# Optimization experiments

Hardware: AMD Instinct MI355X
Metric: run time of the kernel (lower is better)

The kernel has to match this reference:

```python
import jax, jax.numpy as jnp
import numpy as np

HIER = [1, 9, 90, 900, 18000]   # hierchy_struc = get_HTS_strc(...).get_pred_loc()
N = sum(HIER)                    # total time series = attention batch dim
L = len(HIER)                    # levelcount = attention sequence dim
T = 168                          # time_step
HOR = 24                         # horizon
U = 256                          # units[0] = units[1] = units[2] = d_model
NB = 3                           # nblock
NH = 4                           # heads
DK = U // NH


def setup_inputs() -> dict:
    key = jax.random.key(0)
    ks = jax.random.split(key, 10)
    g = lambda k, shape, fan: jax.random.normal(k, shape, jnp.float32) / np.sqrt(fan)
    return {
        "x": jax.random.normal(ks[0], (N, T), jnp.float32),
        "Wl": g(ks[1], (NB, U, T), T),     # fcLSTM (bias=False)
        "Wl1": g(ks[2], (NB, U, U), U),    # fcLSTM1 (bias=False)
        "Wq": g(ks[3], (NB, U, U), U),
        "bq": jnp.zeros((NB, U), jnp.float32),
        "Wk": g(ks[4], (NB, U, U), U),
        "bk": jnp.zeros((NB, U), jnp.float32),
        "Wv": g(ks[5], (NB, U, U), U),
        "bv": jnp.zeros((NB, U), jnp.float32),
        "Wo": g(ks[6], (NB, U, U), U),     # linears[-1] of MultiHeadedAttention
        "bo": jnp.zeros((NB, U), jnp.float32),
        "W20": g(ks[7], (NB, T, U), U),    # fc20 (bias=False)
        "Wfc2": g(ks[8], (HOR, T), T),     # fc2 (bias=False)
        "level_ids": jnp.asarray(np.repeat(np.arange(L), HIER), jnp.int32),
    }


def reference(x, Wl, Wl1, Wq, bq, Wk, bk, Wv, bv, Wo, bo, W20, Wfc2, level_ids):
    softplus = jax.nn.softplus
    n = x.shape[0]
    # get_attmask: TS i (belonging to hierarchy level l) keeps only query row l,
    # applied POST-softmax (mask_matrix=None branch of attention()).
    qmask = jax.nn.one_hot(level_ids, L, dtype=x.dtype)            # (N, L)

    def heads(Y):  # (N, L, U) -> (N, NH, L, DK)
        return Y.reshape(n, L, NH, DK).transpose(0, 2, 1, 3)

    for b in range(NB):
        h = softplus(x @ Wl[b].T)                                  # acf(fcLSTM(x))
        h = softplus(h @ Wl1[b].T)                                 # acf(fcLSTM1(.))
        X = jnp.broadcast_to(h[:, None, :], (n, L, U))             # per-level token stream
        q = heads(X @ Wq[b].T + bq[b])
        k = heads(X @ Wk[b].T + bk[b])
        v = heads(X @ Wv[b].T + bv[b])
        scores = jnp.einsum('nhqd,nhkd->nhqk', q, k) / np.sqrt(DK)  # (N, NH, L, L)
        p = jax.nn.softmax(scores, axis=-1)
        p = p * qmask[:, None, :, None]                             # hierarchical scatter mask
        o = jnp.einsum('nhqk,nhkd->nhqd', p, v)
        o = o.transpose(0, 2, 1, 3).reshape(n, L, U)                # merge heads
        o = o @ Wo[b].T + bo[b]                                     # linears[-1]
        y = o[jnp.arange(n), level_ids]                             # own-level row per TS (N, U)
        x = x + y @ W20[b].T                                        # fc20 + residual, (N, T)
    return x @ Wfc2.T                                               # fc2 -> (N, HOR)
```

## Files before the change

### kernel.cpp

```cpp
#include <hip/hip_runtime.h>
#include <hip/hip_bf16.h>
#include <math.h>

#define N_TS   19000
#define RPB    80
#define NBLKS  238
#define T_DIM  168
#define T_PAD  192
#define U_DIM  256
#define NBLK   3
#define HOR    24

using bf16 = __hip_bfloat16;
typedef short v8s __attribute__((ext_vector_type(8)));
typedef float v4f __attribute__((ext_vector_type(4)));

#define MFMA(a, b, c) __builtin_amdgcn_mfma_f32_16x16x32_bf16((a), (b), (c), 0, 0, 0)

#define BAR() do { asm volatile("s_waitcnt lgkmcnt(0)" ::: "memory"); \
                   __builtin_amdgcn_s_barrier(); } while (0)

__device__ __forceinline__ float softplus_f(float z) {
    return fmaxf(z, 0.0f) + __logf(1.0f + __expf(-fabsf(z)));
}
__device__ __forceinline__ unsigned pack2bf(float a, float b) {
    __hip_bfloat162 t = __float22bfloat162_rn(make_float2(a, b));
    return *(unsigned*)&t;
}
__device__ __forceinline__ short f2bf_s(float x) {
    bf16 h = __float2bfloat16(x); return *(short*)&h;
}
__device__ __forceinline__ v8s make_v8(float4 f0, float4 f1) {
    v8s r;
    r[0] = f2bf_s(f0.x); r[1] = f2bf_s(f0.y); r[2] = f2bf_s(f0.z); r[3] = f2bf_s(f0.w);
    r[4] = f2bf_s(f1.x); r[5] = f2bf_s(f1.y); r[6] = f2bf_s(f1.z); r[7] = f2bf_s(f1.w);
    return r;
}

__global__ __launch_bounds__(256) void wprep(
    const float* __restrict__ Wl, const float* __restrict__ Wl1,
    const float* __restrict__ Wv, const float* __restrict__ bv,
    const float* __restrict__ Wo, const float* __restrict__ bo,
    const float* __restrict__ W20, const float* __restrict__ Wfc2,
    bf16* __restrict__ Wlb, bf16* __restrict__ Wl1b, bf16* __restrict__ Wvob,
    bf16* __restrict__ W20b, bf16* __restrict__ Wfc2b, float* __restrict__ bvo)
{
    const int blk = blockIdx.x, j = threadIdx.x;
    if (blk < 192) {
        const int b = blk / 64, n0 = (blk % 64) * 4;
        const float* wo0 = Wo + (size_t)(b * 256 + n0 + 0) * 256;
        const float* wo1 = Wo + (size_t)(b * 256 + n0 + 1) * 256;
        const float* wo2 = Wo + (size_t)(b * 256 + n0 + 2) * 256;
        const float* wo3 = Wo + (size_t)(b * 256 + n0 + 3) * 256;
        const float* Wv_b = Wv + (size_t)b * 65536;
        float a0 = 0.f, a1 = 0.f, a2 = 0.f, a3 = 0.f;
        #pragma unroll 4
        for (int t = 0; t < 256; ++t) {
            float v = Wv_b[(size_t)t * 256 + j];
            a0 = fmaf(wo0[t], v, a0); a1 = fmaf(wo1[t], v, a1);
            a2 = fmaf(wo2[t], v, a2); a3 = fmaf(wo3[t], v, a3);
        }
        Wvob[(size_t)(b * 256 + n0 + 0) * 256 + j] = __float2bfloat16(a0);
        Wvob[(size_t)(b * 256 + n0 + 1) * 256 + j] = __float2bfloat16(a1);
        Wvob[(size_t)(b * 256 + n0 + 2) * 256 + j] = __float2bfloat16(a2);
        Wvob[(size_t)(b * 256 + n0 + 3) * 256 + j] = __float2bfloat16(a3);

        __shared__ float4 red[256];
        const float bvv = bv[b * 256 + j];
        red[j] = make_float4(wo0[j] * bvv, wo1[j] * bvv, wo2[j] * bvv, wo3[j] * bvv);
        __syncthreads();
        for (int s = 128; s > 0; s >>= 1) {
            if (j < s) {
                float4 x0 = red[j], x1 = red[j + s];
                red[j] = make_float4(x0.x + x1.x, x0.y + x1.y, x0.z + x1.z, x0.w + x1.w);
            }
            __syncthreads();
        }
        if (j == 0) {
            float4 r0 = red[0];
            bvo[b * 256 + n0 + 0] = r0.x + bo[b * 256 + n0 + 0];
            bvo[b * 256 + n0 + 1] = r0.y + bo[b * 256 + n0 + 1];
            bvo[b * 256 + n0 + 2] = r0.z + bo[b * 256 + n0 + 2];
            bvo[b * 256 + n0 + 3] = r0.w + bo[b * 256 + n0 + 3];
        }
    } else if (blk < 960) {
        const int idx = blk - 192, b = idx >> 8, r = idx & 255;
        if (j < T_PAD)
            Wlb[(size_t)(b * 256 + r) * T_PAD + j] =
                __float2bfloat16(j < T_DIM ? Wl[(size_t)(b * 256 + r) * T_DIM + j] : 0.f);
    } else if (blk < 1728) {
        const int idx = blk - 960, b = idx >> 8, r = idx & 255;
        Wl1b[(size_t)(b * 256 + r) * 256 + j] =
            __float2bfloat16(Wl1[(size_t)(b * 256 + r) * 256 + j]);
    } else if (blk < 2304) {
        const int idx = blk - 1728, b = idx / T_PAD, r = idx % T_PAD;
        W20b[(size_t)(b * T_PAD + r) * 256 + j] =
            __float2bfloat16(r < T_DIM ? W20[(size_t)(b * T_DIM + r) * 256 + j] : 0.f);
    } else {
        const int r = blk - 2304;
        if (j < T_PAD)
            Wfc2b[r * T_PAD + j] =
                __float2bfloat16((r < HOR && j < T_DIM) ? Wfc2[r * T_DIM + j] : 0.f);
    }
}

template<int NKS, int NI>
__device__ __forceinline__ void loadW(v8s (&dst)[16], const bf16* __restrict__ W,
                                      int ld, int rowA, int rowB, int kq)
{
    #pragma unroll
    for (int i = 0; i < NI; ++i) {
        const int r = (i == 0) ? rowA : rowB;
        #pragma unroll
        for (int ks = 0; ks < NKS; ++ks)
            dst[i * NKS + ks] = *(const v8s*)&W[(size_t)r * ld + ks * 32 + 8 * kq];
    }
}

template<int NKS, bool SP, bool BIAS>
__device__ __forceinline__ void computeH(const v8s (&wreg)[16],
    const char* src, char* dst, const float* __restrict__ bias,
    int w, int r16, int kq, int swz)
{
    v4f acc[2][5] = {};
    #pragma unroll
    for (int ks = 0; ks < NKS; ++ks)
        #pragma unroll
        for (int j = 0; j < 5; ++j) {
            v8s bfr = *(const v8s*)(src + (16 * j + r16) * 512 + ((64 * ks + 16 * kq) ^ swz));
            acc[0][j] = MFMA(wreg[0 * NKS + ks], bfr, acc[0][j]);
            acc[1][j] = MFMA(wreg[1 * NKS + ks], bfr, acc[1][j]);
        }
    #pragma unroll
    for (int i = 0; i < 2; ++i) {
        const int c0 = 32 * w + 16 * i + 4 * kq;
        float4 bb = make_float4(0.f, 0.f, 0.f, 0.f);
        if (BIAS) bb = *(const float4*)&bias[c0];
        #pragma unroll
        for (int j = 0; j < 5; ++j) {
            float v0 = acc[i][j][0], v1 = acc[i][j][1], v2 = acc[i][j][2], v3 = acc[i][j][3];
            if (BIAS) { v0 += bb.x; v1 += bb.y; v2 += bb.z; v3 += bb.w; }
            if (SP) { v0 = softplus_f(v0); v1 = softplus_f(v1);
                      v2 = softplus_f(v2); v3 = softplus_f(v3); }
            *(uint2*)(dst + (16 * j + r16) * 512 + ((2 * c0) ^ swz)) =
                make_uint2(pack2bf(v0, v1), pack2bf(v2, v3));
        }
    }
}

__global__ __launch_bounds__(512, 2) void fused_net(
    const bf16* __restrict__ Wlb, const bf16* __restrict__ Wl1b,
    const bf16* __restrict__ Wvob, const bf16* __restrict__ W20b,
    const bf16* __restrict__ Wfc2b, const float* __restrict__ bvo,
    const float* __restrict__ x, float* __restrict__ out)
{
    __shared__ __align__(16) bf16  hA[RPB * 256];
    __shared__ __align__(16) bf16  hB[RPB * 256];
    __shared__ __align__(16) float hX[RPB * 192];

    const int tid  = threadIdx.x;
    const int lane = tid & 63, w = tid >> 6;
    const int r16  = lane & 15, kq = lane >> 4;
    const int swz  = (r16 & 7) << 4;
    const int bm   = blockIdx.x * RPB;

    v8s wE[16], wO[16];

    loadW<6, 2>(wE, Wlb, T_PAD, 32 * w + r16, 32 * w + 16 + r16, kq);

    for (int u = tid; u < RPB * 48; u += 512) {
        const int r = u / 48, q = u - r * 48;
        const int gr = bm + r;
        float4 v = make_float4(0.f, 0.f, 0.f, 0.f);
        if (gr < N_TS && q < 42)
            v = *(const float4*)&x[(size_t)gr * T_DIM + 4 * q];
        const int sr = (r & 7) << 4;
        *(float4*)((char*)hX + r * 768 + ((16 * q) ^ sr)) = v;
        *(uint2*)((char*)hB + r * 512 + ((8 * q) ^ sr)) =
            make_uint2(pack2bf(v.x, v.y), pack2bf(v.z, v.w));
    }
    BAR();

    for (int b = 0; b < NBLK; ++b) {
        loadW<8, 2>(wO, Wl1b + (size_t)b * 65536, 256,
                    32 * w + r16, 32 * w + 16 + r16, kq);
        computeH<6, true, false>(wE, (const char*)hB, (char*)hA, nullptr, w, r16, kq, swz);
        BAR();

        loadW<8, 2>(wE, Wvob + (size_t)b * 65536, 256,
                    32 * w + r16, 32 * w + 16 + r16, kq);
        computeH<8, true, false>(wO, (const char*)hA, (char*)hB, nullptr, w, r16, kq, swz);
        BAR();

        {
            const bf16* W4 = W20b + (size_t)b * T_PAD * 256;
            if (w < 4) loadW<8, 2>(wO, W4, 256, 16 * (2 * w) + r16, 16 * (2 * w + 1) + r16, kq);
            else       loadW<8, 1>(wO, W4, 256, 16 * (8 + w - 4) + r16, 0, kq);
        }
        computeH<8, false, true>(wE, (const char*)hB, (char*)hA, bvo + b * 256, w, r16, kq, swz);
        BAR();

        if (b < NBLK - 1) {
            loadW<6, 2>(wE, Wlb + (size_t)(b + 1) * 256 * T_PAD, T_PAD,
                        32 * w + r16, 32 * w + 16 + r16, kq);
        } else {
            #pragma unroll
            for (int ks = 0; ks < 6; ++ks)
                wE[ks] = *(const v8s*)&Wfc2b[(size_t)(16 * (w & 1) + r16) * T_PAD + ks * 32 + 8 * kq];
        }
        {
            const int ti0 = (w < 4) ? 2 * w : 8 + (w - 4);
            v4f acc[2][5] = {};
            #pragma unroll
            for (int ks = 0; ks < 8; ++ks)
                #pragma unroll
                for (int j = 0; j < 5; ++j) {
                    v8s bfr = *(const v8s*)((const char*)hA + (16 * j + r16) * 512 +
                                            ((64 * ks + 16 * kq) ^ swz));
                    acc[0][j] = MFMA(wO[ks], bfr, acc[0][j]);
                    if (w < 4) acc[1][j] = MFMA(wO[8 + ks], bfr, acc[1][j]);
                }
            #pragma unroll
            for (int i = 0; i < 2; ++i) {
                if (i == 1 && w >= 4) continue;
                const int c0 = 16 * (ti0 + i) + 4 * kq;
                #pragma unroll
                for (int j = 0; j < 5; ++j) {
                    const int row = 16 * j + r16;
                    char* pX = (char*)hX + row * 768 + ((4 * c0) ^ swz);
                    float4 v = *(float4*)pX;
                    v.x += acc[i][j][0]; v.y += acc[i][j][1];
                    v.z += acc[i][j][2]; v.w += acc[i][j][3];
                    *(float4*)pX = v;
                    *(uint2*)((char*)hB + row * 512 + ((2 * c0) ^ swz)) =
                        make_uint2(pack2bf(v.x, v.y), pack2bf(v.z, v.w));
                }
            }
        }
        BAR();
    }

    for (int u = w; u < 10; u += 8) {
        const int j = u >> 1;
        v4f acc = {};
        #pragma unroll
        for (int ks = 0; ks < 6; ++ks) {
            const char* base = (const char*)hX + (16 * j + r16) * 768;
            const int   u0   = 128 * ks + 32 * kq;
            float4 f0 = *(const float4*)(base + (u0 ^ swz));
            float4 f1 = *(const float4*)(base + ((u0 + 16) ^ swz));
            v8s xv = make_v8(f0, f1);
            acc = MFMA(wE[ks], xv, acc);
        }
        const int grow = bm + 16 * j + r16;
        const int col  = 16 * (u & 1) + 4 * kq;
        if (grow < N_TS && col < HOR)
            *(float4*)&out[(size_t)grow * HOR + col] =
                make_float4(acc[0], acc[1], acc[2], acc[3]);
    }
}

extern "C" void kernel_launch(void* const* d_in, const int* in_sizes, int n_in,
                              void* d_out, int out_size, void* d_ws, size_t ws_size,
                              hipStream_t stream) {
    const float* x    = (const float*)d_in[0];
    const float* Wl   = (const float*)d_in[1];
    const float* Wl1  = (const float*)d_in[2];
    const float* Wv   = (const float*)d_in[7];
    const float* bv   = (const float*)d_in[8];
    const float* Wo   = (const float*)d_in[9];
    const float* bo   = (const float*)d_in[10];
    const float* W20  = (const float*)d_in[11];
    const float* Wfc2 = (const float*)d_in[12];
    float* out = (float*)d_out;

    char* p = (char*)d_ws;
    auto carve = [&](size_t bytes) { char* q = p; p += (bytes + 255) & ~(size_t)255; return q; };
    bf16*  Wlb   = (bf16*)carve((size_t)NBLK * 256 * T_PAD * 2);
    bf16*  Wl1b  = (bf16*)carve((size_t)NBLK * 256 * 256 * 2);
    bf16*  Wvob  = (bf16*)carve((size_t)NBLK * 256 * 256 * 2);
    bf16*  W20b  = (bf16*)carve((size_t)NBLK * T_PAD * 256 * 2);
    bf16*  Wfc2b = (bf16*)carve((size_t)32 * T_PAD * 2);
    float* bvo   = (float*)carve((size_t)NBLK * 256 * 4);

    wprep<<<dim3(2336), dim3(256), 0, stream>>>(
        Wl, Wl1, Wv, bv, Wo, bo, W20, Wfc2, Wlb, Wl1b, Wvob, W20b, Wfc2b, bvo);
    fused_net<<<dim3(NBLKS), dim3(512), 0, stream>>>(
        Wlb, Wl1b, Wvob, W20b, Wfc2b, bvo, x, out);
}
```

Baseline: 167.8 us.

## Shrink row tile to 32 and drop weight double-buffering for higher occupancy

The per-block row tile drops from 80 to 32 rows, so there are more blocks and less LDS per block. The two weight register buffers (wE/wO) are merged into one, removing the prefetch of the next stage's weights during the current compute. The launch bound is raised to 4 blocks per CU. The aim is to trade the explicit software prefetch for more occupancy to hide latency, but each weight fragment is now reused across fewer rows, so global/L2 weight traffic rises about 2.5x.

```diff
diff --git a/kernel.cpp b/kernel.cpp
--- a/kernel.cpp
+++ b/kernel.cpp
@@ -3,8 +3,8 @@
 #include <math.h>
 
 #define N_TS   19000
-#define RPB    80
-#define NBLKS  238
+#define RPB    32
+#define NBLKS  594
 #define T_DIM  168
 #define T_PAD  192
 #define U_DIM  256
@@ -122,11 +122,11 @@
     const char* src, char* dst, const float* __restrict__ bias,
     int w, int r16, int kq, int swz)
 {
-    v4f acc[2][5] = {};
+    v4f acc[2][2] = {};
     #pragma unroll
     for (int ks = 0; ks < NKS; ++ks)
         #pragma unroll
-        for (int j = 0; j < 5; ++j) {
+        for (int j = 0; j < 2; ++j) {
             v8s bfr = *(const v8s*)(src + (16 * j + r16) * 512 + ((64 * ks + 16 * kq) ^ swz));
             acc[0][j] = MFMA(wreg[0 * NKS + ks], bfr, acc[0][j]);
             acc[1][j] = MFMA(wreg[1 * NKS + ks], bfr, acc[1][j]);
@@ -137,7 +137,7 @@
         float4 bb = make_float4(0.f, 0.f, 0.f, 0.f);
         if (BIAS) bb = *(const float4*)&bias[c0];
         #pragma unroll
-        for (int j = 0; j < 5; ++j) {
+        for (int j = 0; j < 2; ++j) {
             float v0 = acc[i][j][0], v1 = acc[i][j][1], v2 = acc[i][j][2], v3 = acc[i][j][3];
             if (BIAS) { v0 += bb.x; v1 += bb.y; v2 += bb.z; v3 += bb.w; }
             if (SP) { v0 = softplus_f(v0); v1 = softplus_f(v1);
@@ -148,7 +148,7 @@
     }
 }
 
-__global__ __launch_bounds__(512, 2) void fused_net(
+__global__ __launch_bounds__(512, 4) void fused_net(
     const bf16* __restrict__ Wlb, const bf16* __restrict__ Wl1b,
     const bf16* __restrict__ Wvob, const bf16* __restrict__ W20b,
     const bf16* __restrict__ Wfc2b, const float* __restrict__ bvo,
@@ -164,9 +164,7 @@
     const int swz  = (r16 & 7) << 4;
     const int bm   = blockIdx.x * RPB;
 
-    v8s wE[16], wO[16];
-
-    loadW<6, 2>(wE, Wlb, T_PAD, 32 * w + r16, 32 * w + 16 + r16, kq);
+    v8s wreg[16];
 
     for (int u = tid; u < RPB * 48; u += 512) {
         const int r = u / 48, q = u - r * 48;
@@ -182,50 +180,42 @@
     BAR();
 
     for (int b = 0; b < NBLK; ++b) {
-        loadW<8, 2>(wO, Wl1b + (size_t)b * 65536, 256,
+        loadW<6, 2>(wreg, Wlb + (size_t)b * 256 * T_PAD, T_PAD,
                     32 * w + r16, 32 * w + 16 + r16, kq);
-        computeH<6, true, false>(wE, (const char*)hB, (char*)hA, nullptr, w, r16, kq, swz);
-        BAR();
-
-        loadW<8, 2>(wE, Wvob + (size_t)b * 65536, 256,
+        computeH<6, true, false>(wreg, (const char*)hB, (char*)hA, nullptr, w, r16, kq, swz);
+        BAR();
+
+        loadW<8, 2>(wreg, Wl1b + (size_t)b * 65536, 256,
                     32 * w + r16, 32 * w + 16 + r16, kq);
-        computeH<8, true, false>(wO, (const char*)hA, (char*)hB, nullptr, w, r16, kq, swz);
+        computeH<8, true, false>(wreg, (const char*)hA, (char*)hB, nullptr, w, r16, kq, swz);
+        BAR();
+
+        loadW<8, 2>(wreg, Wvob + (size_t)b * 65536, 256,
+                    32 * w + r16, 32 * w + 16 + r16, kq);
+        computeH<8, false, true>(wreg, (const char*)hB, (char*)hA, bvo + b * 256, w, r16, kq, swz);
         BAR();
 
         {
             const bf16* W4 = W20b + (size_t)b * T_PAD * 256;
-            if (w < 4) loadW<8, 2>(wO, W4, 256, 16 * (2 * w) + r16, 16 * (2 * w + 1) + r16, kq);
-            else       loadW<8, 1>(wO, W4, 256, 16 * (8 + w - 4) + r16, 0, kq);
-        }
-        computeH<8, false, true>(wE, (const char*)hB, (char*)hA, bvo + b * 256, w, r16, kq, swz);
-        BAR();
-
-        if (b < NBLK - 1) {
-            loadW<6, 2>(wE, Wlb + (size_t)(b + 1) * 256 * T_PAD, T_PAD,
-                        32 * w + r16, 32 * w + 16 + r16, kq);
-        } else {
-            #pragma unroll
-            for (int ks = 0; ks < 6; ++ks)
-                wE[ks] = *(const v8s*)&Wfc2b[(size_t)(16 * (w & 1) + r16) * T_PAD + ks * 32 + 8 * kq];
-        }
-        {
+            if (w < 4) loadW<8, 2>(wreg, W4, 256, 16 * (2 * w) + r16, 16 * (2 * w + 1) + r16, kq);
+            else       loadW<8, 1>(wreg, W4, 256, 16 * (8 + w - 4) + r16, 0, kq);
             const int ti0 = (w < 4) ? 2 * w : 8 + (w - 4);
-            v4f acc[2][5] = {};
+            v4f acc[2][2] = {};
             #pragma unroll
             for (int ks = 0; ks < 8; ++ks)
                 #pragma unroll
-                for (int j = 0; j < 5; ++j) {
+                for (int j = 0; j < 2; ++j) {
                     v8s bfr = *(const v8s*)((const char*)hA + (16 * j + r16) * 512 +
                                             ((64 * ks + 16 * kq) ^ swz));
-                    acc[0][j] = MFMA(wO[ks], bfr, acc[0][j]);
-                    if (w < 4) acc[1][j] = MFMA(wO[8 + ks], bfr, acc[1][j]);
+                    acc[0][j] = MFMA(wreg[ks], bfr, acc[0][j]);
+                    if (w < 4) acc[1][j] = MFMA(wreg[8 + ks], bfr, acc[1][j]);
                 }
             #pragma unroll
             for (int i = 0; i < 2; ++i) {
                 if (i == 1 && w >= 4) continue;
                 const int c0 = 16 * (ti0 + i) + 4 * kq;
                 #pragma unroll
-                for (int j = 0; j < 5; ++j) {
+                for (int j = 0; j < 2; ++j) {
                     const int row = 16 * j + r16;
                     char* pX = (char*)hX + row * 768 + ((4 * c0) ^ swz);
                     float4 v = *(float4*)pX;
@@ -240,8 +230,8 @@
         BAR();
     }
 
-    for (int u = w; u < 10; u += 8) {
-        const int j = u >> 1;
+    if (w < 4) {
+        const int t = w & 1, j = w >> 1;
         v4f acc = {};
         #pragma unroll
         for (int ks = 0; ks < 6; ++ks) {
@@ -250,10 +240,11 @@
             float4 f0 = *(const float4*)(base + (u0 ^ swz));
             float4 f1 = *(const float4*)(base + ((u0 + 16) ^ swz));
             v8s xv = make_v8(f0, f1);
-            acc = MFMA(wE[ks], xv, acc);
+            v8s a  = *(const v8s*)&Wfc2b[(size_t)(16 * t + r16) * T_PAD + ks * 32 + 8 * kq];
+            acc = MFMA(a, xv, acc);
         }
         const int grow = bm + 16 * j + r16;
-        const int col  = 16 * (u & 1) + 4 * kq;
+        const int col  = 16 * t + 4 * kq;
         if (grow < N_TS && col < HOR)
             *(float4*)&out[(size_t)grow * HOR + col] =
                 make_float4(acc[0], acc[1], acc[2], acc[3]);
```

Result: slower. 232.3 us (+38.4%).
